# Kernel tuning notes

Hardware: AMD Instinct MI355X
Metric: run time of the kernel (lower is better)

## Reference

```python
import jax, jax.numpy as jnp
import numpy as np

H = 50   # hidden_dim (hardcoded in module)
D = 16   # input_dim
B = 4096
T = 512

def _uniform(key, shape, k):
    return jax.random.uniform(key, shape, jnp.float32, -k, k)

def setup_inputs() -> dict:
    key = jax.random.key(0)
    ks = jax.random.split(key, 12)
    k = 1.0 / np.sqrt(H)  # PyTorch LSTM/Linear init bound
    return {
        "x": jax.random.normal(ks[0], (B, T, D), jnp.float32),
        "W_ih0": _uniform(ks[1], (4 * H, D), k),
        "W_hh0": _uniform(ks[2], (4 * H, H), k),
        "b_ih0": _uniform(ks[3], (4 * H,), k),
        "b_hh0": _uniform(ks[4], (4 * H,), k),
        "W_ih1": _uniform(ks[5], (4 * H, H), k),
        "W_hh1": _uniform(ks[6], (4 * H, H), k),
        "b_ih1": _uniform(ks[7], (4 * H,), k),
        "b_hh1": _uniform(ks[8], (4 * H,), k),
        "W_fc": _uniform(ks[9], (1, H), k),
        "b_fc": _uniform(ks[10], (1,), k),
    }

def _lstm_layer(x_tbd, W_ih, W_hh, b):
    # x_tbd: [T, B, Din]; returns (ys [T,B,H], h_final [B,H])
    Bsz = x_tbd.shape[1]
    # precompute input projections for all timesteps: [T, B, 4H]
    xproj = jnp.einsum('tbd,gd->tbg', x_tbd, W_ih) + b

    def step(carry, xp):
        h, c = carry
        gates = xp + h @ W_hh.T  # [B, 4H]
        i, f, g, o = jnp.split(gates, 4, axis=-1)  # torch gate order i,f,g,o
        i = jax.nn.sigmoid(i)
        f = jax.nn.sigmoid(f)
        g = jnp.tanh(g)
        o = jax.nn.sigmoid(o)
        c = f * c + i * g
        h = o * jnp.tanh(c)
        return (h, c), h

    init = (jnp.zeros((Bsz, H), x_tbd.dtype), jnp.zeros((Bsz, H), x_tbd.dtype))
    (h_fin, _), ys = jax.lax.scan(step, init, xproj)
    return ys, h_fin

def reference(x, W_ih0, W_hh0, b_ih0, b_hh0, W_ih1, W_hh1, b_ih1, b_hh1, W_fc, b_fc):
    x_tbd = jnp.transpose(x, (1, 0, 2))  # [T, B, D]
    ys0, _ = _lstm_layer(x_tbd, W_ih0, W_hh0, b_ih0 + b_hh0)
    _, h_n = _lstm_layer(ys0, W_ih1, W_hh1, b_ih1 + b_hh1)
    return h_n @ W_fc.T + b_fc  # [B, 1]
```

## Files before the change

### kernel.cpp

```cpp
#include <hip/hip_runtime.h>


#define TSTEPS 512
#define DIN 16
#define HID 50
#define BPB 16

typedef _Float16 half8 __attribute__((ext_vector_type(8)));
typedef _Float16 half4v __attribute__((ext_vector_type(4)));
typedef __fp16 fp16x2 __attribute__((ext_vector_type(2)));
typedef float f32x4 __attribute__((ext_vector_type(4)));
typedef float f32x2 __attribute__((ext_vector_type(2)));

#define MF(A, B, C) __builtin_amdgcn_mfma_f32_16x16x32_f16((A), (B), (C), 0, 0, 0)

#define HBUF 2304
#define XBUF 1280
#define H0_O 0
#define H1_O 4608
#define X_O  9216
#define SH_BYTES (9216 + 4 * XBUF)

#define BAR() asm volatile("s_waitcnt lgkmcnt(0)\ns_barrier" ::: "memory")

#define NL2E  (-1.4426950408889634f)
#define P2L2E (2.8853900817779268f)

__device__ __forceinline__ unsigned pack2h(float a, float b) {
  union { fp16x2 h; unsigned u; } pk;
  pk.h = __builtin_amdgcn_cvt_pkrtz(a, b);
  return pk.u;
}

__device__ __forceinline__ f32x2 cell2p(const f32x4 gA, const f32x4 gB, f32x2& C) {
  f32x2 gi = {gA[0], gB[0]}, gf = {gA[1], gB[1]};
  f32x2 gg = {gA[2], gB[2]}, go = {gA[3], gB[3]};
  f32x2 ei, ef, eg, eo;
  ei[0] = __builtin_amdgcn_exp2f(gi[0]); ei[1] = __builtin_amdgcn_exp2f(gi[1]);
  ef[0] = __builtin_amdgcn_exp2f(gf[0]); ef[1] = __builtin_amdgcn_exp2f(gf[1]);
  eg[0] = __builtin_amdgcn_exp2f(gg[0]); eg[1] = __builtin_amdgcn_exp2f(gg[1]);
  eo[0] = __builtin_amdgcn_exp2f(fminf(go[0], 30.f));
  eo[1] = __builtin_amdgcn_exp2f(fminf(go[1], 30.f));
  const f32x2 one = {1.f, 1.f};
  const f32x2 c2 = {P2L2E, P2L2E};
  f32x2 a = one + ei, f = one + ef, b = one + eg;
  f32x2 ab = a * b;
  f32x2 f2 = ef * c2 + c2;
  f32x2 t = (eg - one) * f2 + C * ab;
  f32x2 p = f * ab;
  f32x2 rp;
  rp[0] = __builtin_amdgcn_rcpf(p[0]);
  rp[1] = __builtin_amdgcn_rcpf(p[1]);
  C = t * rp;
  f32x2 ec;
  ec[0] = __builtin_amdgcn_exp2f(fminf(C[0], 30.f));
  ec[1] = __builtin_amdgcn_exp2f(fminf(C[1], 30.f));
  f32x2 q = (one + eo) * (one + ec);
  float r2 = __builtin_amdgcn_rcpf(q[0] * q[1]);
  f32x2 h;
  h[0] = (ec[0] - 1.f) * (r2 * q[1]);
  h[1] = (ec[1] - 1.f) * (r2 * q[0]);
  return h;
}

__device__ __forceinline__ half8 load_wfrag(const float* __restrict__ W, int kld,
                                            bool permk, int kreal, int gt, int kt,
                                            int lane, float scale) {
  const int gp = 16 * gt + (lane & 15);
  const int u = gp >> 2, j = gp & 3;
  const int kb = kt * 32 + (lane >> 4) * 8;
  half8 f;
#pragma unroll
  for (int i = 0; i < 8; ++i) {
    const int p = kb + i;
    const int kk = permk ? ((p & ~7) + (((p & 1) << 2) | ((p >> 1) & 3))) : p;
    float v = (u < HID && kk < kreal) ? W[(j * HID + u) * kld + kk] : 0.f;
    f[i] = (_Float16)(v * scale);
  }
  return f;
}

extern "C" __global__ void __launch_bounds__(512, 2)
lstm2_v10(const float* __restrict__ x,
          const float* __restrict__ Wih0, const float* __restrict__ Whh0,
          const float* __restrict__ bih0, const float* __restrict__ bhh0,
          const float* __restrict__ Wih1, const float* __restrict__ Whh1,
          const float* __restrict__ bih1, const float* __restrict__ bhh1,
          const float* __restrict__ Wfc, const float* __restrict__ bfc,
          float* __restrict__ out) {
  __shared__ __align__(16) char sh[SH_BYTES];
  const int tid = threadIdx.x;
  const int lane = tid & 63;
  const int wv = tid >> 6;
  const int bcol = lane & 15;
  const int kg = lane >> 4;
  const int bbase = blockIdx.x * BPB;
  const bool comp = (wv < 7);

  const int sbb = lane >> 2, q = lane & 3;
  const float* xrow = x + ((size_t)(bbase + sbb) * TSTEPS) * DIN + q * 4;

  for (int i = tid; i < SH_BYTES / 4; i += 512) ((int*)sh)[i] = 0;

  const float wsc = ((lane & 3) == 2) ? P2L2E : NL2E;
  half8 w0x[2], w0h[2][2], w1i[2][2], w1h[2][2];
  f32x4 bias0v[2] = {{0,0,0,0},{0,0,0,0}}, bias1v[2] = {{0,0,0,0},{0,0,0,0}};
  if (comp) {
#pragma unroll
    for (int gi = 0; gi < 2; ++gi) {
      const int gt = 2 * wv + gi;
      w0x[gi] = load_wfrag(Wih0, DIN, false, DIN, gt, 0, lane, wsc);
#pragma unroll
      for (int kt = 0; kt < 2; ++kt) {
        w0h[gi][kt] = load_wfrag(Whh0, HID, true, HID, gt, kt, lane, wsc);
        w1i[gi][kt] = load_wfrag(Wih1, HID, true, HID, gt, kt, lane, wsc);
        w1h[gi][kt] = load_wfrag(Whh1, HID, true, HID, gt, kt, lane, wsc);
      }
      const int u = 8 * wv + 4 * gi + kg;
      if (u < HID) {
#pragma unroll
        for (int j = 0; j < 4; ++j) {
          const float bs = (j == 2) ? P2L2E : NL2E;
          bias0v[gi][j] = bs * (bih0[j * HID + u] + bhh0[j * HID + u]);
          bias1v[gi][j] = bs * (bih1[j * HID + u] + bhh1[j * HID + u]);
        }
      }
    }
  }
  f32x2 C0 = {0.f, 0.f}, C1 = {0.f, 0.f};
  const int hoff = bcol * 144 + kg * 16;
  const int xoff = bcol * 80 + kg * 16;
  const int wo32 = bcol * 144 + wv * 16 + kg * 4;

  BAR();

  if (wv == 7) {
#pragma unroll
    for (int t = 0; t < 3; ++t) {
      float4 xq = *(const float4*)(xrow + (size_t)t * DIN);
      half4v h4;
#pragma unroll
      for (int i = 0; i < 4; ++i) h4[i] = (_Float16)((const float*)&xq)[i];
      *(half4v*)(sh + X_O + t * XBUF + sbb * 80 + q * 8) = h4;
    }
  }
  BAR();

  float4 xrA, xrB;
  half8 bxc;
  if (comp) {
    half8 bx0 = *(const half8*)(sh + X_O + 0 * XBUF + xoff);
    bxc = *(const half8*)(sh + X_O + 1 * XBUF + xoff);
    f32x4 a0 = MF(w0x[0], bx0, bias0v[0]);
    f32x4 a1 = MF(w0x[1], bx0, bias0v[1]);
    f32x2 H0 = cell2p(a0, a1, C0);
    *(unsigned*)(sh + H0_O + wo32) = pack2h(H0[0], H0[1]);
  } else if (wv == 7) {
    xrA = *(const float4*)(xrow + (size_t)3 * DIN);
    xrB = *(const float4*)(xrow + (size_t)4 * DIN);
  }
  BAR();

#define STEPCOMP(P, XSN)                                                       \
  do {                                                                         \
    half8 bh0[2], bh1[2];                                                      \
    _Pragma("unroll") for (int kt = 0; kt < 2; ++kt) {                         \
      bh0[kt] = *(const half8*)(sh + H0_O + (P)*HBUF + hoff + kt * 64);        \
      bh1[kt] = *(const half8*)(sh + H1_O + (P)*HBUF + hoff + kt * 64);        \
    }                                                                          \
    half8 bxn = *(const half8*)(sh + X_O + (XSN)*XBUF + xoff);                 \
    f32x4 rv0 = MF(w0x[0], bxc, bias0v[0]);                                    \
    f32x4 rv1 = MF(w0x[1], bxc, bias0v[1]);                                    \
    rv0 = MF(w0h[0][0], bh0[0], rv0);                                          \
    rv1 = MF(w0h[1][0], bh0[0], rv1);                                          \
    rv0 = MF(w0h[0][1], bh0[1], rv0);                                          \
    rv1 = MF(w0h[1][1], bh0[1], rv1);                                          \
    f32x4 qv0 = MF(w1i[0][0], bh0[0], bias1v[0]);                              \
    f32x4 qv1 = MF(w1i[1][0], bh0[0], bias1v[1]);                              \
    qv0 = MF(w1h[0][0], bh1[0], qv0);                                          \
    qv1 = MF(w1h[1][0], bh1[0], qv1);                                          \
    qv0 = MF(w1i[0][1], bh0[1], qv0);                                          \
    qv1 = MF(w1i[1][1], bh0[1], qv1);                                          \
    qv0 = MF(w1h[0][1], bh1[1], qv0);                                          \
    qv1 = MF(w1h[1][1], bh1[1], qv1);                                          \
    f32x2 H0 = cell2p(rv0, rv1, C0);                                           \
    *(unsigned*)(sh + H0_O + ((P) ^ 1) * HBUF + wo32) = pack2h(H0[0], H0[1]);  \
    f32x2 H1 = cell2p(qv0, qv1, C1);                                           \
    *(unsigned*)(sh + H1_O + ((P) ^ 1) * HBUF + wo32) = pack2h(H1[0], H1[1]);  \
    bxc = bxn;                                                                 \
  } while (0)

#define STEPX(T, SLOT, XR)                                                     \
  do {                                                                         \
    half4v h4;                                                                 \
    _Pragma("unroll") for (int i = 0; i < 4; ++i)                              \
        h4[i] = (_Float16)((const float*)&(XR))[i];                            \
    *(half4v*)(sh + X_O + (SLOT)*XBUF + sbb * 80 + q * 8) = h4;                \
    int tl = (T) + 5;                                                          \
    if (tl > TSTEPS - 1) tl = TSTEPS - 1;                                      \
    (XR) = *(const float4*)(xrow + (size_t)tl * DIN);                          \
  } while (0)

  for (int s = 0; s < TSTEPS; s += 4) {
    if (comp) { STEPCOMP(0, 2); } else if (wv == 7) { STEPX(s, 3, xrA); }
    BAR();
    if (comp) { STEPCOMP(1, 3); } else if (wv == 7) { STEPX(s + 1, 0, xrB); }
    BAR();
    if (comp) { STEPCOMP(0, 0); } else if (wv == 7) { STEPX(s + 2, 1, xrA); }
    BAR();
    if (comp) { STEPCOMP(1, 1); } else if (wv == 7) { STEPX(s + 3, 2, xrB); }
    BAR();
  }

  if (tid < BPB) {
    float acc = bfc[0];
#pragma unroll 10
    for (int u = 0; u < HID; ++u) {
      const int pp = (u & ~7) + 2 * (u & 3) + ((u >> 2) & 1);
      float h = (float)(*(const _Float16*)(sh + H1_O + tid * 144 + pp * 2));
      acc = fmaf(Wfc[u], h, acc);
    }
    out[bbase + tid] = acc;
  }
}

extern "C" void kernel_launch(void* const* d_in, const int* in_sizes, int n_in,
                              void* d_out, int out_size, void* d_ws, size_t ws_size,
                              hipStream_t stream) {
  (void)in_sizes; (void)n_in; (void)d_ws; (void)ws_size; (void)out_size;
  lstm2_v10<<<dim3(4096 / BPB), dim3(512), 0, stream>>>(
      (const float*)d_in[0], (const float*)d_in[1], (const float*)d_in[2],
      (const float*)d_in[3], (const float*)d_in[4], (const float*)d_in[5],
      (const float*)d_in[6], (const float*)d_in[7], (const float*)d_in[8],
      (const float*)d_in[9], (const float*)d_in[10], (float*)d_out);
}
```

Baseline: 330.7 us.

## Spread gate tiles across all eight waves and load x directly into registers

New measurement: 370.3 us. 12.0% more time.

```diff
diff --git a/kernel.cpp b/kernel.cpp
--- a/kernel.cpp
+++ b/kernel.cpp
@@ -7,7 +7,6 @@
 #define BPB 16
 
 typedef _Float16 half8 __attribute__((ext_vector_type(8)));
-typedef _Float16 half4v __attribute__((ext_vector_type(4)));
 typedef __fp16 fp16x2 __attribute__((ext_vector_type(2)));
 typedef float f32x4 __attribute__((ext_vector_type(4)));
 typedef float f32x2 __attribute__((ext_vector_type(2)));
@@ -15,11 +14,9 @@
 #define MF(A, B, C) __builtin_amdgcn_mfma_f32_16x16x32_f16((A), (B), (C), 0, 0, 0)
 
 #define HBUF 2304
-#define XBUF 1280
 #define H0_O 0
 #define H1_O 4608
-#define X_O  9216
-#define SH_BYTES (9216 + 4 * XBUF)
+#define SH_BYTES 9216
 
 #define BAR() asm volatile("s_waitcnt lgkmcnt(0)\ns_barrier" ::: "memory")
 
@@ -39,8 +36,7 @@
   ei[0] = __builtin_amdgcn_exp2f(gi[0]); ei[1] = __builtin_amdgcn_exp2f(gi[1]);
   ef[0] = __builtin_amdgcn_exp2f(gf[0]); ef[1] = __builtin_amdgcn_exp2f(gf[1]);
   eg[0] = __builtin_amdgcn_exp2f(gg[0]); eg[1] = __builtin_amdgcn_exp2f(gg[1]);
-  eo[0] = __builtin_amdgcn_exp2f(fminf(go[0], 30.f));
-  eo[1] = __builtin_amdgcn_exp2f(fminf(go[1], 30.f));
+  eo[0] = __builtin_amdgcn_exp2f(go[0]); eo[1] = __builtin_amdgcn_exp2f(go[1]);
   const f32x2 one = {1.f, 1.f};
   const f32x2 c2 = {P2L2E, P2L2E};
   f32x2 a = one + ei, f = one + ef, b = one + eg;
@@ -80,8 +76,27 @@
   return f;
 }
 
+#define LOADX(R0, R1, TT)                                                      \
+  do {                                                                         \
+    int tl_ = (TT);                                                            \
+    if (tl_ > TSTEPS - 1) tl_ = TSTEPS - 1;                                    \
+    const float* p_ = xcol + (size_t)tl_ * DIN;                                \
+    (R0) = *(const float4*)p_;                                                 \
+    (R1) = *(const float4*)(p_ + 4);                                           \
+  } while (0)
+
+#define BXB(BX, R0, R1)                                                        \
+  do {                                                                         \
+    union { half8 h8; fp16x2 p2[4]; } u_;                                      \
+    u_.p2[0] = __builtin_amdgcn_cvt_pkrtz((R0).x, (R0).y);                     \
+    u_.p2[1] = __builtin_amdgcn_cvt_pkrtz((R0).z, (R0).w);                     \
+    u_.p2[2] = __builtin_amdgcn_cvt_pkrtz((R1).x, (R1).y);                     \
+    u_.p2[3] = __builtin_amdgcn_cvt_pkrtz((R1).z, (R1).w);                     \
+    (BX) = u_.h8;                                                              \
+  } while (0)
+
 extern "C" __global__ void __launch_bounds__(512, 2)
-lstm2_v10(const float* __restrict__ x,
+lstm2_v11(const float* __restrict__ x,
           const float* __restrict__ Wih0, const float* __restrict__ Whh0,
           const float* __restrict__ bih0, const float* __restrict__ bhh0,
           const float* __restrict__ Wih1, const float* __restrict__ Whh1,
@@ -95,20 +110,21 @@
   const int bcol = lane & 15;
   const int kg = lane >> 4;
   const int bbase = blockIdx.x * BPB;
-  const bool comp = (wv < 7);
-
-  const int sbb = lane >> 2, q = lane & 3;
-  const float* xrow = x + ((size_t)(bbase + sbb) * TSTEPS) * DIN + q * 4;
+
+  const int nt = (wv < 5) ? 2 : 1;
+  const int gt0 = (wv < 5) ? 2 * wv : (10 + (wv - 5));
+
+  const float* xcol = x + ((size_t)(bbase + bcol)) * TSTEPS * DIN + (kg & 1) * 8;
 
   for (int i = tid; i < SH_BYTES / 4; i += 512) ((int*)sh)[i] = 0;
 
   const float wsc = ((lane & 3) == 2) ? P2L2E : NL2E;
   half8 w0x[2], w0h[2][2], w1i[2][2], w1h[2][2];
   f32x4 bias0v[2] = {{0,0,0,0},{0,0,0,0}}, bias1v[2] = {{0,0,0,0},{0,0,0,0}};
-  if (comp) {
-#pragma unroll
-    for (int gi = 0; gi < 2; ++gi) {
-      const int gt = 2 * wv + gi;
+#pragma unroll
+  for (int gi = 0; gi < 2; ++gi) {
+    if (gi < nt) {
+      const int gt = gt0 + gi;
       w0x[gi] = load_wfrag(Wih0, DIN, false, DIN, gt, 0, lane, wsc);
 #pragma unroll
       for (int kt = 0; kt < 2; ++kt) {
@@ -116,7 +132,7 @@
         w1i[gi][kt] = load_wfrag(Wih1, HID, true, HID, gt, kt, lane, wsc);
         w1h[gi][kt] = load_wfrag(Whh1, HID, true, HID, gt, kt, lane, wsc);
       }
-      const int u = 8 * wv + 4 * gi + kg;
+      const int u = 4 * gt + kg;
       if (u < HID) {
 #pragma unroll
         for (int j = 0; j < 4; ++j) {
@@ -127,88 +143,104 @@
       }
     }
   }
+
   f32x2 C0 = {0.f, 0.f}, C1 = {0.f, 0.f};
   const int hoff = bcol * 144 + kg * 16;
-  const int xoff = bcol * 80 + kg * 16;
-  const int wo32 = bcol * 144 + wv * 16 + kg * 4;
+  const int wo = (nt == 2) ? (bcol * 144 + (gt0 >> 1) * 16 + kg * 4)
+                           : (bcol * 144 + (8 * (gt0 >> 1) + 2 * kg + (gt0 & 1)) * 2);
 
   BAR();
 
-  if (wv == 7) {
-#pragma unroll
-    for (int t = 0; t < 3; ++t) {
-      float4 xq = *(const float4*)(xrow + (size_t)t * DIN);
-      half4v h4;
-#pragma unroll
-      for (int i = 0; i < 4; ++i) h4[i] = (_Float16)((const float*)&xq)[i];
-      *(half4v*)(sh + X_O + t * XBUF + sbb * 80 + q * 8) = h4;
+  float4 a0, a1, b0, b1;
+  LOADX(a0, a1, 0);
+  half8 bx0;
+  BXB(bx0, a0, a1);
+  LOADX(a0, a1, 1);
+  LOADX(b0, b1, 2);
+  {
+    f32x4 r0 = MF(w0x[0], bx0, bias0v[0]);
+    if (nt == 2) {
+      f32x4 r1 = MF(w0x[1], bx0, bias0v[1]);
+      f32x2 H = cell2p(r0, r1, C0);
+      *(unsigned*)(sh + H0_O + wo) = pack2h(H[0], H[1]);
+    } else {
+      f32x2 Cp = {0.f, 0.f};
+      f32x2 H = cell2p(r0, r0, Cp);
+      *(_Float16*)(sh + H0_O + wo) = (_Float16)H[0];
+      C0[0] = 0.f;
+      C0[1] = Cp[0];
     }
   }
   BAR();
 
-  float4 xrA, xrB;
-  half8 bxc;
-  if (comp) {
-    half8 bx0 = *(const half8*)(sh + X_O + 0 * XBUF + xoff);
-    bxc = *(const half8*)(sh + X_O + 1 * XBUF + xoff);
-    f32x4 a0 = MF(w0x[0], bx0, bias0v[0]);
-    f32x4 a1 = MF(w0x[1], bx0, bias0v[1]);
-    f32x2 H0 = cell2p(a0, a1, C0);
-    *(unsigned*)(sh + H0_O + wo32) = pack2h(H0[0], H0[1]);
-  } else if (wv == 7) {
-    xrA = *(const float4*)(xrow + (size_t)3 * DIN);
-    xrB = *(const float4*)(xrow + (size_t)4 * DIN);
-  }
-  BAR();
-
-#define STEPCOMP(P, XSN)                                                       \
+#define STEP2(P, BX)                                                           \
   do {                                                                         \
     half8 bh0[2], bh1[2];                                                      \
     _Pragma("unroll") for (int kt = 0; kt < 2; ++kt) {                         \
       bh0[kt] = *(const half8*)(sh + H0_O + (P)*HBUF + hoff + kt * 64);        \
       bh1[kt] = *(const half8*)(sh + H1_O + (P)*HBUF + hoff + kt * 64);        \
     }                                                                          \
-    half8 bxn = *(const half8*)(sh + X_O + (XSN)*XBUF + xoff);                 \
-    f32x4 rv0 = MF(w0x[0], bxc, bias0v[0]);                                    \
-    f32x4 rv1 = MF(w0x[1], bxc, bias0v[1]);                                    \
-    rv0 = MF(w0h[0][0], bh0[0], rv0);                                          \
-    rv1 = MF(w0h[1][0], bh0[0], rv1);                                          \
-    rv0 = MF(w0h[0][1], bh0[1], rv0);                                          \
-    rv1 = MF(w0h[1][1], bh0[1], rv1);                                          \
-    f32x4 qv0 = MF(w1i[0][0], bh0[0], bias1v[0]);                              \
-    f32x4 qv1 = MF(w1i[1][0], bh0[0], bias1v[1]);                              \
-    qv0 = MF(w1h[0][0], bh1[0], qv0);                                          \
-    qv1 = MF(w1h[1][0], bh1[0], qv1);                                          \
-    qv0 = MF(w1i[0][1], bh0[1], qv0);                                          \
-    qv1 = MF(w1i[1][1], bh0[1], qv1);                                          \
-    qv0 = MF(w1h[0][1], bh1[1], qv0);                                          \
-    qv1 = MF(w1h[1][1], bh1[1], qv1);                                          \
+    const f32x4 z = {0.f, 0.f, 0.f, 0.f};                                      \
+    f32x4 tq0a = MF(w1i[0][0], bh0[0], bias1v[0]);                             \
+    tq0a = MF(w1h[0][0], bh1[0], tq0a);                                        \
+    f32x4 tq0b = MF(w1i[0][1], bh0[1], z);                                     \
+    tq0b = MF(w1h[0][1], bh1[1], tq0b);                                        \
+    f32x4 qv0 = tq0a + tq0b;                                                   \
+    f32x4 tq1a = MF(w1i[1][0], bh0[0], bias1v[1]);                             \
+    tq1a = MF(w1h[1][0], bh1[0], tq1a);                                        \
+    f32x4 tq1b = MF(w1i[1][1], bh0[1], z);                                     \
+    tq1b = MF(w1h[1][1], bh1[1], tq1b);                                        \
+    f32x4 qv1 = tq1a + tq1b;                                                   \
+    f32x4 tr0a = MF(w0x[0], (BX), bias0v[0]);                                  \
+    tr0a = MF(w0h[0][0], bh0[0], tr0a);                                        \
+    f32x4 tr0b = MF(w0h[0][1], bh0[1], z);                                     \
+    f32x4 rv0 = tr0a + tr0b;                                                   \
+    f32x4 tr1a = MF(w0x[1], (BX), bias0v[1]);                                  \
+    tr1a = MF(w0h[1][0], bh0[0], tr1a);                                        \
+    f32x4 tr1b = MF(w0h[1][1], bh0[1], z);                                     \
+    f32x4 rv1 = tr1a + tr1b;                                                   \
+    f32x2 H1 = cell2p(qv0, qv1, C1);                                           \
+    *(unsigned*)(sh + H1_O + ((P) ^ 1) * HBUF + wo) = pack2h(H1[0], H1[1]);    \
     f32x2 H0 = cell2p(rv0, rv1, C0);                                           \
-    *(unsigned*)(sh + H0_O + ((P) ^ 1) * HBUF + wo32) = pack2h(H0[0], H0[1]);  \
-    f32x2 H1 = cell2p(qv0, qv1, C1);                                           \
-    *(unsigned*)(sh + H1_O + ((P) ^ 1) * HBUF + wo32) = pack2h(H1[0], H1[1]);  \
-    bxc = bxn;                                                                 \
-  } while (0)
-
-#define STEPX(T, SLOT, XR)                                                     \
-  do {                                                                         \
-    half4v h4;                                                                 \
-    _Pragma("unroll") for (int i = 0; i < 4; ++i)                              \
-        h4[i] = (_Float16)((const float*)&(XR))[i];                            \
-    *(half4v*)(sh + X_O + (SLOT)*XBUF + sbb * 80 + q * 8) = h4;                \
-    int tl = (T) + 5;                                                          \
-    if (tl > TSTEPS - 1) tl = TSTEPS - 1;                                      \
-    (XR) = *(const float4*)(xrow + (size_t)tl * DIN);                          \
-  } while (0)
-
-  for (int s = 0; s < TSTEPS; s += 4) {
-    if (comp) { STEPCOMP(0, 2); } else if (wv == 7) { STEPX(s, 3, xrA); }
+    *(unsigned*)(sh + H0_O + ((P) ^ 1) * HBUF + wo) = pack2h(H0[0], H0[1]);    \
+  } while (0)
+
+#define STEP1(P, BX)                                                           \
+  do {                                                                         \
+    half8 bh0[2], bh1[2];                                                      \
+    _Pragma("unroll") for (int kt = 0; kt < 2; ++kt) {                         \
+      bh0[kt] = *(const half8*)(sh + H0_O + (P)*HBUF + hoff + kt * 64);        \
+      bh1[kt] = *(const half8*)(sh + H1_O + (P)*HBUF + hoff + kt * 64);        \
+    }                                                                          \
+    const f32x4 z = {0.f, 0.f, 0.f, 0.f};                                      \
+    f32x4 tqa = MF(w1i[0][0], bh0[0], bias1v[0]);                              \
+    tqa = MF(w1h[0][0], bh1[0], tqa);                                          \
+    f32x4 tqb = MF(w1i[0][1], bh0[1], z);                                      \
+    tqb = MF(w1h[0][1], bh1[1], tqb);                                          \
+    f32x4 qv = tqa + tqb;                                                      \
+    f32x4 tra = MF(w0x[0], (BX), bias0v[0]);                                   \
+    tra = MF(w0h[0][0], bh0[0], tra);                                          \
+    f32x4 trb = MF(w0h[0][1], bh0[1], z);                                      \
+    f32x4 rv = tra + trb;                                                      \
+    f32x2 H = cell2p(qv, rv, C0);                                              \
+    *(_Float16*)(sh + H1_O + ((P) ^ 1) * HBUF + wo) = (_Float16)H[0];          \
+    *(_Float16*)(sh + H0_O + ((P) ^ 1) * HBUF + wo) = (_Float16)H[1];          \
+  } while (0)
+
+  for (int s = 0; s < TSTEPS; s += 2) {
+    {
+      half8 bxA;
+      BXB(bxA, a0, a1);
+      LOADX(a0, a1, s + 3);
+      if (nt == 2) { STEP2(0, bxA); } else { STEP1(0, bxA); }
+    }
     BAR();
-    if (comp) { STEPCOMP(1, 3); } else if (wv == 7) { STEPX(s + 1, 0, xrB); }
-    BAR();
-    if (comp) { STEPCOMP(0, 0); } else if (wv == 7) { STEPX(s + 2, 1, xrA); }
-    BAR();
-    if (comp) { STEPCOMP(1, 1); } else if (wv == 7) { STEPX(s + 3, 2, xrB); }
+    {
+      half8 bxB;
+      BXB(bxB, b0, b1);
+      LOADX(b0, b1, s + 4);
+      if (nt == 2) { STEP2(1, bxB); } else { STEP1(1, bxB); }
+    }
     BAR();
   }
 
@@ -228,7 +260,7 @@
                               void* d_out, int out_size, void* d_ws, size_t ws_size,
                               hipStream_t stream) {
   (void)in_sizes; (void)n_in; (void)d_ws; (void)ws_size; (void)out_size;
-  lstm2_v10<<<dim3(4096 / BPB), dim3(512), 0, stream>>>(
+  lstm2_v11<<<dim3(4096 / BPB), dim3(512), 0, stream>>>(
       (const float*)d_in[0], (const float*)d_in[1], (const float*)d_in[2],
       (const float*)d_in[3], (const float*)d_in[4], (const float*)d_in[5],
       (const float*)d_in[6], (const float*)d_in[7], (const float*)d_in[8],
```

## Split LSTM gate work across 13 compute waves with one gate tile each

Applied to the files above, without the earlier changes.

Result: no change. 332.5 us (+0.6%).

```diff
diff --git a/kernel.cpp b/kernel.cpp
--- a/kernel.cpp
+++ b/kernel.cpp
@@ -25,12 +25,6 @@
 
 #define NL2E  (-1.4426950408889634f)
 #define P2L2E (2.8853900817779268f)
-
-__device__ __forceinline__ unsigned pack2h(float a, float b) {
-  union { fp16x2 h; unsigned u; } pk;
-  pk.h = __builtin_amdgcn_cvt_pkrtz(a, b);
-  return pk.u;
-}
 
 __device__ __forceinline__ f32x2 cell2p(const f32x4 gA, const f32x4 gB, f32x2& C) {
   f32x2 gi = {gA[0], gB[0]}, gf = {gA[1], gB[1]};
@@ -39,8 +33,7 @@
   ei[0] = __builtin_amdgcn_exp2f(gi[0]); ei[1] = __builtin_amdgcn_exp2f(gi[1]);
   ef[0] = __builtin_amdgcn_exp2f(gf[0]); ef[1] = __builtin_amdgcn_exp2f(gf[1]);
   eg[0] = __builtin_amdgcn_exp2f(gg[0]); eg[1] = __builtin_amdgcn_exp2f(gg[1]);
-  eo[0] = __builtin_amdgcn_exp2f(fminf(go[0], 30.f));
-  eo[1] = __builtin_amdgcn_exp2f(fminf(go[1], 30.f));
+  eo[0] = __builtin_amdgcn_exp2f(go[0]); eo[1] = __builtin_amdgcn_exp2f(go[1]);
   const f32x2 one = {1.f, 1.f};
   const f32x2 c2 = {P2L2E, P2L2E};
   f32x2 a = one + ei, f = one + ef, b = one + eg;
@@ -80,8 +73,8 @@
   return f;
 }
 
-extern "C" __global__ void __launch_bounds__(512, 2)
-lstm2_v10(const float* __restrict__ x,
+extern "C" __global__ void __launch_bounds__(896, 1)
+lstm2_v14(const float* __restrict__ x,
           const float* __restrict__ Wih0, const float* __restrict__ Whh0,
           const float* __restrict__ bih0, const float* __restrict__ bhh0,
           const float* __restrict__ Wih1, const float* __restrict__ Whh1,
@@ -95,46 +88,44 @@
   const int bcol = lane & 15;
   const int kg = lane >> 4;
   const int bbase = blockIdx.x * BPB;
-  const bool comp = (wv < 7);
+  const bool comp = (wv < 13);
+  const int gt = wv;
 
   const int sbb = lane >> 2, q = lane & 3;
   const float* xrow = x + ((size_t)(bbase + sbb) * TSTEPS) * DIN + q * 4;
 
-  for (int i = tid; i < SH_BYTES / 4; i += 512) ((int*)sh)[i] = 0;
+  for (int i = tid; i < SH_BYTES / 4; i += 896) ((int*)sh)[i] = 0;
 
   const float wsc = ((lane & 3) == 2) ? P2L2E : NL2E;
-  half8 w0x[2], w0h[2][2], w1i[2][2], w1h[2][2];
-  f32x4 bias0v[2] = {{0,0,0,0},{0,0,0,0}}, bias1v[2] = {{0,0,0,0},{0,0,0,0}};
+  half8 w0x, w0h[2], w1i[2], w1h[2];
+  f32x4 bias0v = {0, 0, 0, 0}, bias1v = {0, 0, 0, 0};
   if (comp) {
-#pragma unroll
-    for (int gi = 0; gi < 2; ++gi) {
-      const int gt = 2 * wv + gi;
-      w0x[gi] = load_wfrag(Wih0, DIN, false, DIN, gt, 0, lane, wsc);
-#pragma unroll
-      for (int kt = 0; kt < 2; ++kt) {
-        w0h[gi][kt] = load_wfrag(Whh0, HID, true, HID, gt, kt, lane, wsc);
-        w1i[gi][kt] = load_wfrag(Wih1, HID, true, HID, gt, kt, lane, wsc);
-        w1h[gi][kt] = load_wfrag(Whh1, HID, true, HID, gt, kt, lane, wsc);
+    w0x = load_wfrag(Wih0, DIN, false, DIN, gt, 0, lane, wsc);
+#pragma unroll
+    for (int kt = 0; kt < 2; ++kt) {
+      w0h[kt] = load_wfrag(Whh0, HID, true, HID, gt, kt, lane, wsc);
+      w1i[kt] = load_wfrag(Wih1, HID, true, HID, gt, kt, lane, wsc);
+      w1h[kt] = load_wfrag(Whh1, HID, true, HID, gt, kt, lane, wsc);
+    }
+    const int u = 4 * gt + kg;
+    if (u < HID) {
+#pragma unroll
+      for (int j = 0; j < 4; ++j) {
+        const float bs = (j == 2) ? P2L2E : NL2E;
+        bias0v[j] = bs * (bih0[j * HID + u] + bhh0[j * HID + u]);
+        bias1v[j] = bs * (bih1[j * HID + u] + bhh1[j * HID + u]);
       }
-      const int u = 8 * wv + 4 * gi + kg;
-      if (u < HID) {
-#pragma unroll
-        for (int j = 0; j < 4; ++j) {
-          const float bs = (j == 2) ? P2L2E : NL2E;
-          bias0v[gi][j] = bs * (bih0[j * HID + u] + bhh0[j * HID + u]);
-          bias1v[gi][j] = bs * (bih1[j * HID + u] + bhh1[j * HID + u]);
-        }
-      }
-    }
-  }
-  f32x2 C0 = {0.f, 0.f}, C1 = {0.f, 0.f};
+    }
+  }
+
+  f32x2 C = {0.f, 0.f};
   const int hoff = bcol * 144 + kg * 16;
   const int xoff = bcol * 80 + kg * 16;
-  const int wo32 = bcol * 144 + wv * 16 + kg * 4;
+  const int wo_s = bcol * 144 + (8 * (gt >> 1) + 2 * kg + (gt & 1)) * 2;
 
   BAR();
 
-  if (wv == 7) {
+  if (wv == 13) {
 #pragma unroll
     for (int t = 0; t < 3; ++t) {
       float4 xq = *(const float4*)(xrow + (size_t)t * DIN);
@@ -151,17 +142,19 @@
   if (comp) {
     half8 bx0 = *(const half8*)(sh + X_O + 0 * XBUF + xoff);
     bxc = *(const half8*)(sh + X_O + 1 * XBUF + xoff);
-    f32x4 a0 = MF(w0x[0], bx0, bias0v[0]);
-    f32x4 a1 = MF(w0x[1], bx0, bias0v[1]);
-    f32x2 H0 = cell2p(a0, a1, C0);
-    *(unsigned*)(sh + H0_O + wo32) = pack2h(H0[0], H0[1]);
-  } else if (wv == 7) {
+    f32x4 r0 = MF(w0x, bx0, bias0v);
+    f32x2 Cp = {0.f, 0.f};
+    f32x2 Hs = cell2p(r0, r0, Cp);
+    *(_Float16*)(sh + H0_O + wo_s) = (_Float16)Hs[0];
+    C[0] = 0.f;
+    C[1] = Cp[0];
+  } else if (wv == 13) {
     xrA = *(const float4*)(xrow + (size_t)3 * DIN);
     xrB = *(const float4*)(xrow + (size_t)4 * DIN);
   }
   BAR();
 
-#define STEPCOMP(P, XSN)                                                       \
+#define STEPC(P, XSN)                                                          \
   do {                                                                         \
     half8 bh0[2], bh1[2];                                                      \
     _Pragma("unroll") for (int kt = 0; kt < 2; ++kt) {                         \
@@ -169,24 +162,16 @@
       bh1[kt] = *(const half8*)(sh + H1_O + (P)*HBUF + hoff + kt * 64);        \
     }                                                                          \
     half8 bxn = *(const half8*)(sh + X_O + (XSN)*XBUF + xoff);                 \
-    f32x4 rv0 = MF(w0x[0], bxc, bias0v[0]);                                    \
-    f32x4 rv1 = MF(w0x[1], bxc, bias0v[1]);                                    \
-    rv0 = MF(w0h[0][0], bh0[0], rv0);                                          \
-    rv1 = MF(w0h[1][0], bh0[0], rv1);                                          \
-    rv0 = MF(w0h[0][1], bh0[1], rv0);                                          \
-    rv1 = MF(w0h[1][1], bh0[1], rv1);                                          \
-    f32x4 qv0 = MF(w1i[0][0], bh0[0], bias1v[0]);                              \
-    f32x4 qv1 = MF(w1i[1][0], bh0[0], bias1v[1]);                              \
-    qv0 = MF(w1h[0][0], bh1[0], qv0);                                          \
-    qv1 = MF(w1h[1][0], bh1[0], qv1);                                          \
-    qv0 = MF(w1i[0][1], bh0[1], qv0);                                          \
-    qv1 = MF(w1i[1][1], bh0[1], qv1);                                          \
-    qv0 = MF(w1h[0][1], bh1[1], qv0);                                          \
-    qv1 = MF(w1h[1][1], bh1[1], qv1);                                          \
-    f32x2 H0 = cell2p(rv0, rv1, C0);                                           \
-    *(unsigned*)(sh + H0_O + ((P) ^ 1) * HBUF + wo32) = pack2h(H0[0], H0[1]);  \
-    f32x2 H1 = cell2p(qv0, qv1, C1);                                           \
-    *(unsigned*)(sh + H1_O + ((P) ^ 1) * HBUF + wo32) = pack2h(H1[0], H1[1]);  \
+    f32x4 qv = MF(w1i[0], bh0[0], bias1v);                                     \
+    qv = MF(w1h[0], bh1[0], qv);                                               \
+    qv = MF(w1i[1], bh0[1], qv);                                               \
+    qv = MF(w1h[1], bh1[1], qv);                                               \
+    f32x4 rv = MF(w0x, bxc, bias0v);                                           \
+    rv = MF(w0h[0], bh0[0], rv);                                               \
+    rv = MF(w0h[1], bh0[1], rv);                                               \
+    f32x2 Hs = cell2p(qv, rv, C);                                              \
+    *(_Float16*)(sh + H1_O + ((P) ^ 1) * HBUF + wo_s) = (_Float16)Hs[0];       \
+    *(_Float16*)(sh + H0_O + ((P) ^ 1) * HBUF + wo_s) = (_Float16)Hs[1];       \
     bxc = bxn;                                                                 \
   } while (0)
 
@@ -202,13 +187,13 @@
   } while (0)
 
   for (int s = 0; s < TSTEPS; s += 4) {
-    if (comp) { STEPCOMP(0, 2); } else if (wv == 7) { STEPX(s, 3, xrA); }
-    BAR();
-    if (comp) { STEPCOMP(1, 3); } else if (wv == 7) { STEPX(s + 1, 0, xrB); }
-    BAR();
-    if (comp) { STEPCOMP(0, 0); } else if (wv == 7) { STEPX(s + 2, 1, xrA); }
-    BAR();
-    if (comp) { STEPCOMP(1, 1); } else if (wv == 7) { STEPX(s + 3, 2, xrB); }
+    if (comp) { STEPC(0, 2); } else if (wv == 13) { STEPX(s, 3, xrA); }
+    BAR();
+    if (comp) { STEPC(1, 3); } else if (wv == 13) { STEPX(s + 1, 0, xrB); }
+    BAR();
+    if (comp) { STEPC(0, 0); } else if (wv == 13) { STEPX(s + 2, 1, xrA); }
+    BAR();
+    if (comp) { STEPC(1, 1); } else if (wv == 13) { STEPX(s + 3, 2, xrB); }
     BAR();
   }
 
@@ -228,7 +213,7 @@
                               void* d_out, int out_size, void* d_ws, size_t ws_size,
                               hipStream_t stream) {
   (void)in_sizes; (void)n_in; (void)d_ws; (void)ws_size; (void)out_size;
-  lstm2_v10<<<dim3(4096 / BPB), dim3(512), 0, stream>>>(
+  lstm2_v14<<<dim3(4096 / BPB), dim3(896), 0, stream>>>(
       (const float*)d_in[0], (const float*)d_in[1], (const float*)d_in[2],
       (const float*)d_in[3], (const float*)d_in[4], (const float*)d_in[5],
       (const float*)d_in[6], (const float*)d_in[7], (const float*)d_in[8],
```
